# Performance work log

Measured on AMD Instinct MI355X. Metric: run time of the kernel, lower is better.

## Reference

```python
import jax, jax.numpy as jnp
import numpy as np

N_NODES = 100000
N_FEAT = 512
N_HID = 256
N_EDGES = 3200000


def setup_inputs() -> dict:
    key = jax.random.key(0)
    ks = jax.random.split(key, 8)
    x_1 = jax.random.normal(ks[0], (1, N_NODES, N_FEAT), dtype=jnp.float32)
    x_2 = jax.random.normal(ks[1], (1, N_NODES, N_FEAT), dtype=jnp.float32)
    edge_index = jax.random.randint(ks[2], (2, N_EDGES), 0, N_NODES, dtype=jnp.int64)
    edge_vals = jax.random.uniform(ks[3], (N_EDGES,), dtype=jnp.float32)
    # xavier_normal for fc weight [n_hidden, n_features]
    fc_std = float(np.sqrt(2.0 / (N_FEAT + N_HID)))
    fc_w = jax.random.normal(ks[4], (N_HID, N_FEAT), dtype=jnp.float32) * fc_std
    fc_b = jnp.zeros((N_HID,), dtype=jnp.float32)
    prelu_a = jnp.full((1,), 0.25, dtype=jnp.float32)
    bil_std = float(np.sqrt(2.0 / (N_HID + N_HID)))
    bil_w = jax.random.normal(ks[5], (1, N_HID, N_HID), dtype=jnp.float32) * bil_std
    bil_b = jnp.zeros((1,), dtype=jnp.float32)
    return {"x_1": x_1, "x_2": x_2, "edge_vals": edge_vals, "fc_w": fc_w,
            "fc_b": fc_b, "prelu_a": prelu_a, "bil_w": bil_w, "bil_b": bil_b,
            "edge_index": edge_index}


def _gcn(x, edge_index, edge_vals, fc_w, fc_b, prelu_a):
    # x: [1, N, F] -> linear -> spmm(adj, h) -> PReLU
    h = jnp.einsum('bnf,hf->bnh', x, fc_w) + fc_b  # [1, N, H]
    row, col = edge_index[0], edge_index[1]
    msgs = edge_vals[:, None] * h[0, col]          # gather source features [E, H]
    agg = jax.ops.segment_sum(msgs, row, num_segments=N_NODES)  # [N, H]
    agg = agg[None]                                 # [1, N, H]
    return jnp.where(agg >= 0, agg, prelu_a[0] * agg)


def reference(x_1, x_2, edge_vals, fc_w, fc_b, prelu_a, bil_w, bil_b, edge_index):
    h_1 = _gcn(x_1, edge_index, edge_vals, fc_w, fc_b, prelu_a)  # [1, N, H]
    h_2 = _gcn(x_2, edge_index, edge_vals, fc_w, fc_b, prelu_a)  # [1, N, H]
    s = jax.nn.sigmoid(jnp.mean(h_1, axis=1))  # [1, H]
    # Bilinear(n_h, n_h, 1): score[n] = h[n] @ W[0] @ s + b
    v = jnp.einsum('ohg,bg->bh', bil_w, s)      # [1, H]
    score_1 = jnp.einsum('bnh,bh->bn', h_1, v) + bil_b[0]  # [1, N]
    score_2 = jnp.einsum('bnh,bh->bn', h_2, v) + bil_b[0]  # [1, N]
    return jnp.concatenate([score_1, score_2], axis=1)  # [1, 2N]
```

## Files before the change

### kernel.cpp

```cpp
#include <hip/hip_runtime.h>
#include <hip/hip_bf16.h>

#define N_NODES 100000
#define N_FEAT  512
#define N_HID   256
#define N_EDGES 3200000

typedef __attribute__((ext_vector_type(8))) short bf16x8;
typedef __attribute__((ext_vector_type(4))) float f32x4;

__device__ __forceinline__ unsigned short bfu(float f)
{
    __hip_bfloat16 b = __float2bfloat16(f);
    return *(unsigned short*)&b;
}

__device__ __forceinline__ void llds16(const void* g, void* l)
{
    __builtin_amdgcn_global_load_lds(
        (const __attribute__((address_space(1))) unsigned int*)g,
        (__attribute__((address_space(3))) unsigned int*)l,
        16, 0, 0);
}

__global__ __launch_bounds__(256) void convert_bf16_kernel(
    const float* __restrict__ in, unsigned short* __restrict__ outp, int n8)
{
    const int i = blockIdx.x * 256 + threadIdx.x;
    if (i >= n8) return;
    const float4 v0 = *(const float4*)(in + (size_t)i * 8);
    const float4 v1 = *(const float4*)(in + (size_t)i * 8 + 4);
    union { unsigned short s[8]; uint4 u; } pk;
    pk.s[0] = bfu(v0.x); pk.s[1] = bfu(v0.y); pk.s[2] = bfu(v0.z); pk.s[3] = bfu(v0.w);
    pk.s[4] = bfu(v1.x); pk.s[5] = bfu(v1.y); pk.s[6] = bfu(v1.z); pk.s[7] = bfu(v1.w);
    *(uint4*)(outp + (size_t)i * 8) = pk.u;
}

#define BM 64
#define BN 256
#define BK 32

__global__ __launch_bounds__(256) void gemm_mfma(
    const float* __restrict__ X, const unsigned short* __restrict__ Wb,
    const float* __restrict__ bias, unsigned short* __restrict__ Hout, int N)
{
    __shared__ unsigned short As[BM * BK];
    __shared__ unsigned short Bs[BN * BK];

    const int tid  = threadIdx.x;
    const int wave = tid >> 6;
    const int lane = tid & 63;
    const int m0   = blockIdx.x * BM;

    int arow = m0 + (tid >> 2);
    if (arow >= N) arow = N - 1;
    const float* ag = X + (size_t)arow * N_FEAT + (tid & 3) * 8;
    unsigned short* a_dst = As + tid * 8;

    const unsigned short* bg = Wb + (size_t)(tid >> 2) * N_FEAT + (tid & 3) * 8;

    const unsigned short* ap = As + (lane & 15) * BK + (lane >> 4) * 8;
    const unsigned short* bp = Bs + ((size_t)(wave * 64 + (lane & 15))) * BK + (lane >> 4) * 8;

    f32x4 acc[4][4] = {};

    for (int k0 = 0; k0 < N_FEAT; k0 += BK) {
        if (k0) __syncthreads();
        #pragma unroll
        for (int i = 0; i < 4; i++)
            llds16(bg + (size_t)i * 64 * N_FEAT + k0, Bs + ((size_t)(i * 256 + tid)) * 8);
        const float4 x0 = *(const float4*)(ag + k0);
        const float4 x1 = *(const float4*)(ag + k0 + 4);
        union { unsigned short s[8]; uint4 u; } pk;
        pk.s[0] = bfu(x0.x); pk.s[1] = bfu(x0.y); pk.s[2] = bfu(x0.z); pk.s[3] = bfu(x0.w);
        pk.s[4] = bfu(x1.x); pk.s[5] = bfu(x1.y); pk.s[6] = bfu(x1.z); pk.s[7] = bfu(x1.w);
        *(uint4*)a_dst = pk.u;
        __syncthreads();

        bf16x8 af[4], bfr[4];
        #pragma unroll
        for (int mt = 0; mt < 4; mt++) af[mt] = *(const bf16x8*)(ap + mt * 16 * BK);
        #pragma unroll
        for (int nt = 0; nt < 4; nt++) bfr[nt] = *(const bf16x8*)(bp + nt * 16 * BK);
        #pragma unroll
        for (int mt = 0; mt < 4; mt++)
            #pragma unroll
            for (int nt = 0; nt < 4; nt++)
                acc[mt][nt] = __builtin_amdgcn_mfma_f32_16x16x32_bf16(
                    af[mt], bfr[nt], acc[mt][nt], 0, 0, 0);
    }

    const int q  = lane >> 4;
    const int c0 = lane & 15;
    float bcol[4];
    #pragma unroll
    for (int nt = 0; nt < 4; nt++) bcol[nt] = bias[wave * 64 + nt * 16 + c0];
    #pragma unroll
    for (int mt = 0; mt < 4; mt++) {
        #pragma unroll
        for (int r = 0; r < 4; r++) {
            const int row = m0 + mt * 16 + q * 4 + r;
            if (row >= N) continue;
            #pragma unroll
            for (int nt = 0; nt < 4; nt++) {
                const int col = wave * 64 + nt * 16 + c0;
                Hout[(size_t)row * N_HID + col] = bfu(acc[mt][nt][r] + bcol[nt]);
            }
        }
    }
}

__global__ __launch_bounds__(256) void histogram_rows(
    const int* __restrict__ rows, int* __restrict__ counts, int E)
{
    const int e = blockIdx.x * 256 + threadIdx.x;
    if (e < E) atomicAdd(&counts[rows[e]], 1);
}

#define SCAN_T 1024
__global__ __launch_bounds__(SCAN_T) void scan_kernel(
    const int* __restrict__ counts, int* __restrict__ offsets, int n)
{
    const int tid = threadIdx.x;
    const int seg = (n + SCAN_T - 1) / SCAN_T;
    const int s0 = tid * seg;
    const int s1 = min(s0 + seg, n);

    int sum = 0;
    for (int i = s0; i < s1; i++) sum += counts[i];

    __shared__ int wsum[SCAN_T / 64];
    const int lane = tid & 63;
    const int wid  = tid >> 6;
    int v = sum;
    #pragma unroll
    for (int off = 1; off < 64; off <<= 1) {
        int t = __shfl_up(v, off);
        if (lane >= off) v += t;
    }
    if (lane == 63) wsum[wid] = v;
    __syncthreads();
    if (wid == 0 && lane < SCAN_T / 64) {
        int w = wsum[lane];
        #pragma unroll
        for (int off = 1; off < SCAN_T / 64; off <<= 1) {
            int t = __shfl_up(w, off);
            if (lane >= off) w += t;
        }
        wsum[lane] = w;
    }
    __syncthreads();
    int base = v - sum + (wid > 0 ? wsum[wid - 1] : 0);

    int run = base;
    for (int i = s0; i < s1; i++) {
        const int c = counts[i];
        offsets[i] = run;
        run += c;
    }
    if (tid == SCAN_T - 1) offsets[n] = run;
}

__global__ __launch_bounds__(256) void scatter_edges(
    const int* __restrict__ rows, const int* __restrict__ cols,
    const float* __restrict__ ev, int* __restrict__ cursor,
    int2* __restrict__ ecv, int E)
{
    const int e = blockIdx.x * 256 + threadIdx.x;
    if (e >= E) return;
    const int pos = atomicAdd(&cursor[rows[e]], 1);
    int2 p;
    p.x = cols[e];
    p.y = __float_as_int(ev[e]);
    ecv[pos] = p;
}

__device__ __forceinline__ void bf4_unpack(uint2 raw, float& f0, float& f1,
                                           float& f2, float& f3)
{
    f0 = __uint_as_float(raw.x << 16);
    f1 = __uint_as_float(raw.x & 0xffff0000u);
    f2 = __uint_as_float(raw.y << 16);
    f3 = __uint_as_float(raw.y & 0xffff0000u);
}

__device__ __forceinline__ uint2 bf4_pack(float f0, float f1, float f2, float f3)
{
    union { unsigned short u[4]; uint2 v; } pk;
    pk.u[0] = bfu(f0); pk.u[1] = bfu(f1); pk.u[2] = bfu(f2); pk.u[3] = bfu(f3);
    return pk.v;
}

__global__ __launch_bounds__(256) void agg_rows_1(
    const __hip_bfloat16* __restrict__ H, const int* __restrict__ offsets,
    const int2* __restrict__ ecv, const float* __restrict__ pa,
    __hip_bfloat16* __restrict__ hpost, int N)
{
    const int row = blockIdx.x * 4 + (threadIdx.x >> 6);
    if (row >= N) return;
    const int lane = threadIdx.x & 63;
    const int beg = offsets[row], end = offsets[row + 1];
    const unsigned short* Hs = (const unsigned short*)H;

    float a0 = 0.f, a1 = 0.f, a2 = 0.f, a3 = 0.f;
    int e = beg;
    for (; e + 3 < end; e += 4) {
        const int2 p0 = ecv[e], p1 = ecv[e + 1], p2 = ecv[e + 2], p3 = ecv[e + 3];
        const uint2 r0 = *(const uint2*)(Hs + (size_t)p0.x * N_HID + lane * 4);
        const uint2 r1 = *(const uint2*)(Hs + (size_t)p1.x * N_HID + lane * 4);
        const uint2 r2 = *(const uint2*)(Hs + (size_t)p2.x * N_HID + lane * 4);
        const uint2 r3 = *(const uint2*)(Hs + (size_t)p3.x * N_HID + lane * 4);
        const float v0 = __int_as_float(p0.y), v1 = __int_as_float(p1.y);
        const float v2 = __int_as_float(p2.y), v3 = __int_as_float(p3.y);
        float f0, f1, f2, f3;
        bf4_unpack(r0, f0, f1, f2, f3);
        a0 += v0 * f0; a1 += v0 * f1; a2 += v0 * f2; a3 += v0 * f3;
        bf4_unpack(r1, f0, f1, f2, f3);
        a0 += v1 * f0; a1 += v1 * f1; a2 += v1 * f2; a3 += v1 * f3;
        bf4_unpack(r2, f0, f1, f2, f3);
        a0 += v2 * f0; a1 += v2 * f1; a2 += v2 * f2; a3 += v2 * f3;
        bf4_unpack(r3, f0, f1, f2, f3);
        a0 += v3 * f0; a1 += v3 * f1; a2 += v3 * f2; a3 += v3 * f3;
    }
    for (; e < end; e++) {
        const int2 p0 = ecv[e];
        const float v0 = __int_as_float(p0.y);
        const uint2 r0 = *(const uint2*)(Hs + (size_t)p0.x * N_HID + lane * 4);
        float f0, f1, f2, f3;
        bf4_unpack(r0, f0, f1, f2, f3);
        a0 += v0 * f0; a1 += v0 * f1; a2 += v0 * f2; a3 += v0 * f3;
    }
    const float al = pa[0];
    a0 = (a0 >= 0.f) ? a0 : al * a0;
    a1 = (a1 >= 0.f) ? a1 : al * a1;
    a2 = (a2 >= 0.f) ? a2 : al * a2;
    a3 = (a3 >= 0.f) ? a3 : al * a3;
    *(uint2*)((unsigned short*)hpost + (size_t)row * N_HID + lane * 4) =
        bf4_pack(a0, a1, a2, a3);
}

__global__ __launch_bounds__(256) void agg_rows_2(
    const __hip_bfloat16* __restrict__ H, const int* __restrict__ offsets,
    const int2* __restrict__ ecv, const float* __restrict__ pa,
    const float* __restrict__ vbuf, const float* __restrict__ bilb,
    float* __restrict__ out, int N)
{
    __shared__ float vs[N_HID];
    vs[threadIdx.x] = vbuf[threadIdx.x];
    __syncthreads();

    const int row = blockIdx.x * 4 + (threadIdx.x >> 6);
    if (row >= N) return;
    const int lane = threadIdx.x & 63;
    const int beg = offsets[row], end = offsets[row + 1];
    const unsigned short* Hs = (const unsigned short*)H;

    float a0 = 0.f, a1 = 0.f, a2 = 0.f, a3 = 0.f;
    int e = beg;
    for (; e + 3 < end; e += 4) {
        const int2 p0 = ecv[e], p1 = ecv[e + 1], p2 = ecv[e + 2], p3 = ecv[e + 3];
        const uint2 r0 = *(const uint2*)(Hs + (size_t)p0.x * N_HID + lane * 4);
        const uint2 r1 = *(const uint2*)(Hs + (size_t)p1.x * N_HID + lane * 4);
        const uint2 r2 = *(const uint2*)(Hs + (size_t)p2.x * N_HID + lane * 4);
        const uint2 r3 = *(const uint2*)(Hs + (size_t)p3.x * N_HID + lane * 4);
        const float v0 = __int_as_float(p0.y), v1 = __int_as_float(p1.y);
        const float v2 = __int_as_float(p2.y), v3 = __int_as_float(p3.y);
        float f0, f1, f2, f3;
        bf4_unpack(r0, f0, f1, f2, f3);
        a0 += v0 * f0; a1 += v0 * f1; a2 += v0 * f2; a3 += v0 * f3;
        bf4_unpack(r1, f0, f1, f2, f3);
        a0 += v1 * f0; a1 += v1 * f1; a2 += v1 * f2; a3 += v1 * f3;
        bf4_unpack(r2, f0, f1, f2, f3);
        a0 += v2 * f0; a1 += v2 * f1; a2 += v2 * f2; a3 += v2 * f3;
        bf4_unpack(r3, f0, f1, f2, f3);
        a0 += v3 * f0; a1 += v3 * f1; a2 += v3 * f2; a3 += v3 * f3;
    }
    for (; e < end; e++) {
        const int2 p0 = ecv[e];
        const float v0 = __int_as_float(p0.y);
        const uint2 r0 = *(const uint2*)(Hs + (size_t)p0.x * N_HID + lane * 4);
        float f0, f1, f2, f3;
        bf4_unpack(r0, f0, f1, f2, f3);
        a0 += v0 * f0; a1 += v0 * f1; a2 += v0 * f2; a3 += v0 * f3;
    }
    const float al = pa[0];
    a0 = (a0 >= 0.f) ? a0 : al * a0;
    a1 = (a1 >= 0.f) ? a1 : al * a1;
    a2 = (a2 >= 0.f) ? a2 : al * a2;
    a3 = (a3 >= 0.f) ? a3 : al * a3;

    float p = a0 * vs[lane * 4 + 0] + a1 * vs[lane * 4 + 1] +
              a2 * vs[lane * 4 + 2] + a3 * vs[lane * 4 + 3];
    #pragma unroll
    for (int off = 32; off > 0; off >>= 1) p += __shfl_down(p, off);
    if (lane == 0) out[row] = p + bilb[0];
}

#define NPB 256
__global__ __launch_bounds__(256) void colsum_kernel(
    const __hip_bfloat16* __restrict__ hpost, float* __restrict__ colsum, int N)
{
    const int j = threadIdx.x;
    const int n0 = blockIdx.x * NPB;
    const int n1 = min(n0 + NPB, N);
    float s = 0.f;
    for (int n = n0; n < n1; n++)
        s += __bfloat162float(hpost[(size_t)n * N_HID + j]);
    atomicAdd(&colsum[j], s);
}

__global__ __launch_bounds__(256) void compute_v(
    const float* __restrict__ colsum, const float* __restrict__ bilw,
    float* __restrict__ vbuf, int N)
{
    __shared__ float s[N_HID];
    const int t = threadIdx.x;
    const float mean = colsum[t] / (float)N;
    s[t] = 1.f / (1.f + expf(-mean));
    __syncthreads();
    float acc = 0.f;
    #pragma unroll 4
    for (int g = 0; g < N_HID; g++) acc += bilw[t * N_HID + g] * s[g];
    vbuf[t] = acc;
}

__global__ __launch_bounds__(256) void score_kernel(
    const __hip_bfloat16* __restrict__ hpost, const float* __restrict__ vbuf,
    const float* __restrict__ bilb, float* __restrict__ out, int N)
{
    __shared__ float vs[N_HID];
    vs[threadIdx.x] = vbuf[threadIdx.x];
    __syncthreads();
    const int n = blockIdx.x * 4 + (threadIdx.x >> 6);
    if (n >= N) return;
    const int lane = threadIdx.x & 63;
    const uint2 raw = *(const uint2*)((const unsigned short*)hpost +
                                      (size_t)n * N_HID + lane * 4);
    float f0, f1, f2, f3;
    bf4_unpack(raw, f0, f1, f2, f3);
    float p = f0 * vs[lane * 4 + 0] + f1 * vs[lane * 4 + 1] +
              f2 * vs[lane * 4 + 2] + f3 * vs[lane * 4 + 3];
    #pragma unroll
    for (int off = 32; off > 0; off >>= 1) p += __shfl_down(p, off);
    if (lane == 0) out[n] = p + bilb[0];
}

extern "C" void kernel_launch(void* const* d_in, const int* in_sizes, int n_in,
                              void* d_out, int out_size, void* d_ws, size_t ws_size,
                              hipStream_t stream)
{
    const float* x1     = (const float*)d_in[0];
    const float* x2     = (const float*)d_in[1];
    const float* evals  = (const float*)d_in[2];
    const float* fc_w   = (const float*)d_in[3];
    const float* fc_b   = (const float*)d_in[4];
    const float* prelua = (const float*)d_in[5];
    const float* bil_w  = (const float*)d_in[6];
    const float* bil_b  = (const float*)d_in[7];
    const int*   eidx   = (const int*)d_in[8];
    const int*   erow   = eidx;
    const int*   ecol   = eidx + N_EDGES;
    float* out = (float*)d_out;

    char* ws = (char*)d_ws;
    __hip_bfloat16* h_bf   = (__hip_bfloat16*)(ws);
    __hip_bfloat16* hpost1 = (__hip_bfloat16*)(ws + (size_t)52 * 1000000);
    int2*  ecv    = (int2*) (ws + (size_t)104 * 1000000);
    unsigned short* wbf = (unsigned short*)(ws + (size_t)130 * 1000000);
    int*   counts = (int*)  (ws + (size_t)131 * 1000000);
    int*   offs   = (int*)  (ws + (size_t)131500000);
    int*   cursor = (int*)  (ws + (size_t)132 * 1000000);
    float* colsum = (float*)(ws + (size_t)132500000);
    float* vbuf   = colsum + N_HID;

    const int gemm_blocks = (N_NODES + BM - 1) / BM;
    const int eblocks   = (N_EDGES + 255) / 256;
    const int rowblocks = (N_NODES + 3) / 4;
    const int csblocks  = (N_NODES + NPB - 1) / NPB;

    hipMemsetAsync(counts, 0, N_NODES * sizeof(int), stream);
    hipMemsetAsync(colsum, 0, N_HID * sizeof(float), stream);
    histogram_rows<<<eblocks, 256, 0, stream>>>(erow, counts, N_EDGES);
    scan_kernel<<<1, SCAN_T, 0, stream>>>(counts, offs, N_NODES);
    hipMemcpyAsync(cursor, offs, N_NODES * sizeof(int),
                   hipMemcpyDeviceToDevice, stream);
    scatter_edges<<<eblocks, 256, 0, stream>>>(erow, ecol, evals, cursor,
                                               ecv, N_EDGES);
    convert_bf16_kernel<<<(N_HID * N_FEAT / 8 + 255) / 256, 256, 0, stream>>>(
        fc_w, wbf, N_HID * N_FEAT / 8);

    gemm_mfma<<<gemm_blocks, 256, 0, stream>>>(x1, wbf, fc_b,
                                               (unsigned short*)h_bf, N_NODES);
    agg_rows_1<<<rowblocks, 256, 0, stream>>>(h_bf, offs, ecv, prelua,
                                              hpost1, N_NODES);
    colsum_kernel<<<csblocks, 256, 0, stream>>>(hpost1, colsum, N_NODES);
    compute_v<<<1, 256, 0, stream>>>(colsum, bil_w, vbuf, N_NODES);
    score_kernel<<<rowblocks, 256, 0, stream>>>(hpost1, vbuf, bil_b, out, N_NODES);

    gemm_mfma<<<gemm_blocks, 256, 0, stream>>>(x2, wbf, fc_b,
                                               (unsigned short*)h_bf, N_NODES);
    agg_rows_2<<<rowblocks, 256, 0, stream>>>(h_bf, offs, ecv, prelua,
                                              vbuf, bil_b, out + N_NODES, N_NODES);
}
```

Measured before the change: 1.549 ms.

## Build CSR with sub-bucketed ranks instead of second atomic scatter pass

Edges now get a rank in a first atomic pass over per-row sub-buckets (four per row, chosen by edge index), which spreads atomic contention on each counter. The scatter pass then computes its position from the scanned offsets plus the saved rank, with no second atomic pass and no cursor copy. The cost is a scan over four times as many counters, still done by a single block, plus a rank array that is written and read back. Counts and ranks are placed in workspace reused by the bf16 H buffer, which is written only later.

```diff
diff --git a/kernel.cpp b/kernel.cpp
--- a/kernel.cpp
+++ b/kernel.cpp
@@ -5,6 +5,9 @@
 #define N_FEAT  512
 #define N_HID   256
 #define N_EDGES 3200000
+
+#define KREP 4
+#define NB2  (N_NODES * KREP)
 
 typedef __attribute__((ext_vector_type(8))) short bf16x8;
 typedef __attribute__((ext_vector_type(4))) float f32x4;
@@ -110,11 +113,14 @@
     }
 }
 
-__global__ __launch_bounds__(256) void histogram_rows(
-    const int* __restrict__ rows, int* __restrict__ counts, int E)
+__global__ __launch_bounds__(256) void rank_pass(
+    const int* __restrict__ rows, int* __restrict__ counts2,
+    int* __restrict__ rank, int E)
 {
     const int e = blockIdx.x * 256 + threadIdx.x;
-    if (e < E) atomicAdd(&counts[rows[e]], 1);
+    if (e >= E) return;
+    const int b = rows[e] * KREP + (e & (KREP - 1));
+    rank[e] = atomicAdd(&counts2[b], 1);
 }
 
 #define SCAN_T 1024
@@ -163,12 +169,13 @@
 
 __global__ __launch_bounds__(256) void scatter_edges(
     const int* __restrict__ rows, const int* __restrict__ cols,
-    const float* __restrict__ ev, int* __restrict__ cursor,
-    int2* __restrict__ ecv, int E)
+    const float* __restrict__ ev, const int* __restrict__ rank,
+    const int* __restrict__ offs2, int2* __restrict__ ecv, int E)
 {
     const int e = blockIdx.x * 256 + threadIdx.x;
     if (e >= E) return;
-    const int pos = atomicAdd(&cursor[rows[e]], 1);
+    const int b = rows[e] * KREP + (e & (KREP - 1));
+    const int pos = offs2[b] + rank[e];
     int2 p;
     p.x = cols[e];
     p.y = __float_as_int(ev[e]);
@@ -192,14 +199,14 @@
 }
 
 __global__ __launch_bounds__(256) void agg_rows_1(
-    const __hip_bfloat16* __restrict__ H, const int* __restrict__ offsets,
+    const __hip_bfloat16* __restrict__ H, const int* __restrict__ offs2,
     const int2* __restrict__ ecv, const float* __restrict__ pa,
     __hip_bfloat16* __restrict__ hpost, int N)
 {
     const int row = blockIdx.x * 4 + (threadIdx.x >> 6);
     if (row >= N) return;
     const int lane = threadIdx.x & 63;
-    const int beg = offsets[row], end = offsets[row + 1];
+    const int beg = offs2[row * KREP], end = offs2[row * KREP + KREP];
     const unsigned short* Hs = (const unsigned short*)H;
 
     float a0 = 0.f, a1 = 0.f, a2 = 0.f, a3 = 0.f;
@@ -240,7 +247,7 @@
 }
 
 __global__ __launch_bounds__(256) void agg_rows_2(
-    const __hip_bfloat16* __restrict__ H, const int* __restrict__ offsets,
+    const __hip_bfloat16* __restrict__ H, const int* __restrict__ offs2,
     const int2* __restrict__ ecv, const float* __restrict__ pa,
     const float* __restrict__ vbuf, const float* __restrict__ bilb,
     float* __restrict__ out, int N)
@@ -252,7 +259,7 @@
     const int row = blockIdx.x * 4 + (threadIdx.x >> 6);
     if (row >= N) return;
     const int lane = threadIdx.x & 63;
-    const int beg = offsets[row], end = offsets[row + 1];
+    const int beg = offs2[row * KREP], end = offs2[row * KREP + KREP];
     const unsigned short* Hs = (const unsigned short*)H;
 
     float a0 = 0.f, a1 = 0.f, a2 = 0.f, a3 = 0.f;
@@ -367,31 +374,29 @@
     __hip_bfloat16* hpost1 = (__hip_bfloat16*)(ws + (size_t)52 * 1000000);
     int2*  ecv    = (int2*) (ws + (size_t)104 * 1000000);
     unsigned short* wbf = (unsigned short*)(ws + (size_t)130 * 1000000);
-    int*   counts = (int*)  (ws + (size_t)131 * 1000000);
-    int*   offs   = (int*)  (ws + (size_t)131500000);
-    int*   cursor = (int*)  (ws + (size_t)132 * 1000000);
-    float* colsum = (float*)(ws + (size_t)132500000);
+    int*   offs2  = (int*)  (ws + (size_t)130400000);
+    float* colsum = (float*)(ws + (size_t)132100000);
     float* vbuf   = colsum + N_HID;
+    int*   counts2 = (int*)(ws);
+    int*   rank    = (int*)(ws + (size_t)4000000);
 
     const int gemm_blocks = (N_NODES + BM - 1) / BM;
     const int eblocks   = (N_EDGES + 255) / 256;
     const int rowblocks = (N_NODES + 3) / 4;
     const int csblocks  = (N_NODES + NPB - 1) / NPB;
 
-    hipMemsetAsync(counts, 0, N_NODES * sizeof(int), stream);
+    hipMemsetAsync(counts2, 0, NB2 * sizeof(int), stream);
     hipMemsetAsync(colsum, 0, N_HID * sizeof(float), stream);
-    histogram_rows<<<eblocks, 256, 0, stream>>>(erow, counts, N_EDGES);
-    scan_kernel<<<1, SCAN_T, 0, stream>>>(counts, offs, N_NODES);
-    hipMemcpyAsync(cursor, offs, N_NODES * sizeof(int),
-                   hipMemcpyDeviceToDevice, stream);
-    scatter_edges<<<eblocks, 256, 0, stream>>>(erow, ecol, evals, cursor,
-                                               ecv, N_EDGES);
+    rank_pass<<<eblocks, 256, 0, stream>>>(erow, counts2, rank, N_EDGES);
+    scan_kernel<<<1, SCAN_T, 0, stream>>>(counts2, offs2, NB2);
+    scatter_edges<<<eblocks, 256, 0, stream>>>(erow, ecol, evals, rank,
+                                               offs2, ecv, N_EDGES);
     convert_bf16_kernel<<<(N_HID * N_FEAT / 8 + 255) / 256, 256, 0, stream>>>(
         fc_w, wbf, N_HID * N_FEAT / 8);
 
     gemm_mfma<<<gemm_blocks, 256, 0, stream>>>(x1, wbf, fc_b,
                                                (unsigned short*)h_bf, N_NODES);
-    agg_rows_1<<<rowblocks, 256, 0, stream>>>(h_bf, offs, ecv, prelua,
+    agg_rows_1<<<rowblocks, 256, 0, stream>>>(h_bf, offs2, ecv, prelua,
                                               hpost1, N_NODES);
     colsum_kernel<<<csblocks, 256, 0, stream>>>(hpost1, colsum, N_NODES);
     compute_v<<<1, 256, 0, stream>>>(colsum, bil_w, vbuf, N_NODES);
@@ -399,6 +404,6 @@
 
     gemm_mfma<<<gemm_blocks, 256, 0, stream>>>(x2, wbf, fc_b,
                                                (unsigned short*)h_bf, N_NODES);
-    agg_rows_2<<<rowblocks, 256, 0, stream>>>(h_bf, offs, ecv, prelua,
+    agg_rows_2<<<rowblocks, 256, 0, stream>>>(h_bf, offs2, ecv, prelua,
                                               vbuf, bil_b, out + N_NODES, N_NODES);
 }
```

Result: slower. 1.884 ms (+21.6%).
